# Kernel optimization log

Measured on AMD Instinct MI355X. Metric: run time of the kernel, lower is better.

## Reference

```python
import jax, jax.numpy as jnp
import numpy as np

B, C, H, W = 4, 256, 64, 64
CK = C // 8  # query/key channels per OUT_RATIO=8


def setup_inputs() -> dict:
    key = jax.random.key(0)
    ks = jax.random.split(key, 8)
    s_in = 1.0 / np.sqrt(C)
    return {
        "x": jax.random.normal(ks[0], (B, C, H, W), dtype=jnp.float32),
        "Wq": jax.random.uniform(ks[1], (CK, C), jnp.float32, -s_in, s_in),
        "bq": jax.random.uniform(ks[2], (CK,), jnp.float32, -s_in, s_in),
        "Wk": jax.random.uniform(ks[3], (CK, C), jnp.float32, -s_in, s_in),
        "bk": jax.random.uniform(ks[4], (CK,), jnp.float32, -s_in, s_in),
        "Wv": jax.random.uniform(ks[5], (C, C), jnp.float32, -s_in, s_in),
        "bv": jax.random.uniform(ks[6], (C,), jnp.float32, -s_in, s_in),
        "gamma": jnp.zeros((1,), dtype=jnp.float32),
    }


def reference(x, Wq, bq, Wk, bk, Wv, bv, gamma):
    b, c, h, w = x.shape
    n = h * w
    xf = x.reshape(b, c, n)  # [B, C, N]
    # 1x1 convs are channel matmuls
    q = jnp.einsum('oc,bcn->bno', Wq, xf) + bq  # [B, N, CK]
    k = jnp.einsum('oc,bcn->bon', Wk, xf) + bk[None, :, None]  # [B, CK, N]
    v = jnp.einsum('oc,bcn->bon', Wv, xf) + bv[None, :, None]  # [B, C, N]
    energy = jnp.einsum('bno,bom->bnm', q, k)  # [B, N, N], unscaled
    attn = jax.nn.softmax(energy, axis=-1)
    out = jnp.einsum('bcm,bnm->bcn', v, attn)  # [B, C, N]
    out = out.reshape(b, c, h, w)
    return gamma[0] * out + x
```

## Files before the change

kernel.cpp:

```cpp
#include <hip/hip_runtime.h>
#include <math.h>


#define BB 4
#define CC 256
#define NN 4096
#define CKK 32
#define LOG2E 1.44269504f

typedef __attribute__((ext_vector_type(4))) float f32x4;
typedef __attribute__((ext_vector_type(16))) float f32x16;
typedef __attribute__((ext_vector_type(8))) short short8;
typedef __attribute__((ext_vector_type(4))) short short4v;

static __device__ __forceinline__ ushort f2bf(float f) {
    union { float f; unsigned u; } v; v.f = f;
    unsigned r = v.u + 0x7FFFu + ((v.u >> 16) & 1u);
    return (ushort)(r >> 16);
}
static __device__ __forceinline__ float bf2f(ushort h) {
    union { unsigned u; float f; } v; v.u = ((unsigned)h) << 16;
    return v.f;
}
static __device__ __forceinline__ unsigned pack2(float lo, float hi) {
    unsigned r;
    asm("v_cvt_pk_bf16_f32 %0, %1, %2" : "=v"(r) : "v"(lo), "v"(hi));
    return r;
}
static __device__ __forceinline__ float exp2fast(float x) {
    return __builtin_amdgcn_exp2f(x);
}
static __device__ __forceinline__ void gload_lds16(const void* g, void* l) {
    __builtin_amdgcn_global_load_lds(
        (const __attribute__((address_space(1))) void*)g,
        (__attribute__((address_space(3))) void*)l, 16, 0, 0);
}

__global__ __launch_bounds__(256) void pack_w_kernel(
    const float* __restrict__ Wq, const float* __restrict__ bq,
    const float* __restrict__ Wk, const float* __restrict__ bk,
    const float* __restrict__ Wv, const float* __restrict__ bv,
    ushort* __restrict__ Wb, float* __restrict__ bias)
{
    const int o = blockIdx.x;
    const int c = threadIdx.x;
    const float* src; float bsc;
    if (o < 32)      { src = Wq + o * CC;        bsc = bq[o]; }
    else if (o < 64) { src = Wk + (o - 32) * CC; bsc = bk[o - 32]; }
    else             { src = Wv + (o - 64) * CC; bsc = bv[o - 64]; }
    Wb[o * CC + c] = f2bf(src[c]);
    if (c == 0) bias[o] = bsc;
}

__global__ __launch_bounds__(256) void qkv_mfma_kernel(
    const ushort* __restrict__ Wb, const float* __restrict__ bias,
    const float* __restrict__ x,
    ushort* __restrict__ Q, ushort* __restrict__ Kt, ushort* __restrict__ Vg)
{
    const int b = blockIdx.y, n0 = blockIdx.x * 64;
    const int tid = threadIdx.x;
    const int w = tid >> 6, lane = tid & 63, l15 = lane & 15, q = lane >> 4;

    f32x4 acc[5][4];
    #pragma unroll
    for (int c5 = 0; c5 < 5; ++c5)
        #pragma unroll
        for (int nc = 0; nc < 4; ++nc) acc[c5][nc] = (f32x4)0.f;

    const float* xb = x + (size_t)b * CC * NN + n0;

    #pragma unroll
    for (int ks = 0; ks < 8; ++ks) {
        short8 af[5];
        #pragma unroll
        for (int c5 = 0; c5 < 5; ++c5)
            af[c5] = *(const short8*)&Wb[(w * 80 + c5 * 16 + l15) * CC + ks * 32 + q * 8];
        union { unsigned u[4]; short8 v; } bfu[4];
        #pragma unroll
        for (int nc = 0; nc < 4; ++nc) {
            const float* xp = xb + (size_t)(ks * 32 + q * 8) * NN + nc * 16 + l15;
            bfu[nc].u[0] = pack2(xp[0],              xp[(size_t)NN]);
            bfu[nc].u[1] = pack2(xp[2 * (size_t)NN], xp[3 * (size_t)NN]);
            bfu[nc].u[2] = pack2(xp[4 * (size_t)NN], xp[5 * (size_t)NN]);
            bfu[nc].u[3] = pack2(xp[6 * (size_t)NN], xp[7 * (size_t)NN]);
        }
        #pragma unroll
        for (int c5 = 0; c5 < 5; ++c5)
            #pragma unroll
            for (int nc = 0; nc < 4; ++nc)
                acc[c5][nc] = __builtin_amdgcn_mfma_f32_16x16x32_bf16(af[c5], bfu[nc].v, acc[c5][nc], 0, 0, 0);
    }

    const int kh2b = (l15 >> 2) & 1;
    const int jj   = (l15 & 3) + ((l15 >> 3) << 2);

    #pragma unroll
    for (int c5 = 0; c5 < 5; ++c5) {
        const int o0 = w * 80 + c5 * 16;
        float bia[4];
        #pragma unroll
        for (int r = 0; r < 4; ++r) bia[r] = bias[o0 + q * 4 + r];
        if (o0 >= 64) {
            #pragma unroll
            for (int nc = 0; nc < 4; ++nc) {
                const size_t tbase =
                    ((size_t)b * (NN / 32) + (n0 >> 5) + (nc >> 1)) * 8192
                    + (size_t)(((nc & 1) << 1) + kh2b) * 2048 + jj;
                #pragma unroll
                for (int r = 0; r < 4; ++r) {
                    const int c = o0 - 64 + q * 4 + r;
                    Vg[tbase + c * 8] = f2bf(acc[c5][nc][r] + bia[r]);
                }
            }
        } else {
            ushort* dst = (o0 < 32) ? Q : Kt;
            const float sc = (o0 < 32) ? LOG2E : 1.0f;
            const int oo = (o0 & 31) + q * 4;
            #pragma unroll
            for (int nc = 0; nc < 4; ++nc) {
                short4v h;
                #pragma unroll
                for (int r = 0; r < 4; ++r) h[r] = (short)f2bf((acc[c5][nc][r] + bia[r]) * sc);
                *(short4v*)&dst[((size_t)b * NN + n0 + nc * 16 + l15) * CKK + oo] = h;
            }
        }
    }
}

__global__ __launch_bounds__(256, 2) void attn_mfma_kernel(
    const ushort* __restrict__ Q, const ushort* __restrict__ K,
    const ushort* __restrict__ Vg,
    ushort* __restrict__ Op, float* __restrict__ Mp, float* __restrict__ Lp,
    int G, int NSEG)
{
    __shared__ __align__(16) ushort vs[2][16384];

    const int id = blockIdx.x;
    const int xcd = id & 7, ix = id >> 3;
    const int b = xcd >> 1;
    int g, row;
    if (G == 4) { g = ((xcd & 1) << 1) | (ix & 1); row = ix >> 1; }
    else        { g = xcd & 1;                     row = ix; }
    const int n0 = row * 128;

    const int tid = threadIdx.x;
    const int w = tid >> 6, lane = tid & 63;
    const int l31 = lane & 31, h2 = lane >> 5;
    const int n0w = n0 + w * 32;

    const size_t qrow = ((size_t)b * NN + n0w + l31) * CKK;
    short8 qB0 = *(const short8*)&Q[qrow + h2 * 8];
    short8 qB1 = *(const short8*)&Q[qrow + 16 + h2 * 8];

    f32x16 acc[8];
    #pragma unroll
    for (int cb = 0; cb < 8; ++cb) acc[cb] = (f32x16)0.f;
    float m_i = -3.0e38f, l_p = 0.f;

    const int m_start = g * NSEG;
    const int NT = NSEG / 64;
    const ushort* Kb = K + (size_t)b * NN * CKK;
    const char* Vseg = (const char*)Vg
        + ((size_t)b * (NN / 32) + (size_t)(m_start >> 5)) * 16384;

    const int goff = (w << 10) + (lane << 4);
    const int loff = (w << 10);

    #pragma unroll
    for (int i = 0; i < 8; ++i)
        gload_lds16(Vseg + (i << 12) + goff, (char*)&vs[0][0] + (i << 12) + loff);

    short8 kA0 = *(const short8*)&Kb[(size_t)(m_start + l31) * CKK + h2 * 8];
    short8 kA1 = *(const short8*)&Kb[(size_t)(m_start + l31) * CKK + 16 + h2 * 8];
    f32x16 s = __builtin_amdgcn_mfma_f32_32x32x16_bf16(kA0, qB0, (f32x16)0.f, 0, 0, 0);
    s = __builtin_amdgcn_mfma_f32_32x32x16_bf16(kA1, qB1, s, 0, 0, 0);
    {
        const int m1 = m_start + ((NSEG > 32) ? 32 : 0);
        kA0 = *(const short8*)&Kb[(size_t)(m1 + l31) * CKK + h2 * 8];
        kA1 = *(const short8*)&Kb[(size_t)(m1 + l31) * CKK + 16 + h2 * 8];
    }
    __syncthreads();

    int cur = 0;
    for (int t = 0; t < NT; ++t) {
        const char* Vtn = Vseg + (size_t)((t + 1 < NT) ? t + 1 : 0) * 32768;
        #pragma unroll
        for (int i = 0; i < 8; ++i)
            gload_lds16(Vtn + (i << 12) + goff, (char*)&vs[cur ^ 1][0] + (i << 12) + loff);

        #pragma unroll
        for (int sub = 0; sub < 2; ++sub) {
            const int u = 2 * t + sub;

            f32x16 sn = __builtin_amdgcn_mfma_f32_32x32x16_bf16(kA0, qB0, (f32x16)0.f, 0, 0, 0);
            sn = __builtin_amdgcn_mfma_f32_32x32x16_bf16(kA1, qB1, sn, 0, 0, 0);
            const int mo2 = (u + 2) * 32;
            const int m2 = m_start + ((mo2 < NSEG) ? mo2 : 0);
            kA0 = *(const short8*)&Kb[(size_t)(m2 + l31) * CKK + h2 * 8];
            kA1 = *(const short8*)&Kb[(size_t)(m2 + l31) * CKK + 16 + h2 * 8];

            float t0 = fmaxf(fmaxf(s[0],  s[1]),  s[2]);
            float t1 = fmaxf(fmaxf(s[3],  s[4]),  s[5]);
            float t2 = fmaxf(fmaxf(s[6],  s[7]),  s[8]);
            float t3 = fmaxf(fmaxf(s[9],  s[10]), s[11]);
            float t4 = fmaxf(fmaxf(s[12], s[13]), s[14]);
            float mx = fmaxf(fmaxf(fmaxf(t0, t1), t2), fmaxf(fmaxf(t3, t4), s[15]));
            mx = fmaxf(mx, __shfl_xor(mx, 32));
            const bool resc = mx > m_i + 8.f;
            const float mn = resc ? mx : m_i;
            const float al = resc ? exp2fast(m_i - mx) : 1.f;
            union { unsigned uu[8]; short8 v[2]; } P;
            float sum0 = 0.f, sum1 = 0.f;
            #pragma unroll
            for (int g2 = 0; g2 < 8; ++g2) {
                const float plo = exp2fast(s[2 * g2]     - mn);
                const float phi = exp2fast(s[2 * g2 + 1] - mn);
                if (g2 & 1) sum1 += plo + phi; else sum0 += plo + phi;
                P.uu[g2] = pack2(plo, phi);
            }
            l_p = l_p * al + (sum0 + sum1);
            m_i = mn;
            if (__any(resc)) {
                #pragma unroll
                for (int cb = 0; cb < 8; ++cb) acc[cb] *= al;
            }

            const ushort* vsub = &vs[cur][sub * 8192];
            __builtin_amdgcn_s_setprio(1);
            #pragma unroll
            for (int cb = 0; cb < 8; ++cb) {
                const short8 A0 = *(const short8*)&vsub[(size_t)h2 * 2048       + (cb * 32 + l31) * 8];
                const short8 A1 = *(const short8*)&vsub[(size_t)(2 + h2) * 2048 + (cb * 32 + l31) * 8];
                acc[cb] = __builtin_amdgcn_mfma_f32_32x32x16_bf16(A0, P.v[0], acc[cb], 0, 0, 0);
                acc[cb] = __builtin_amdgcn_mfma_f32_32x32x16_bf16(A1, P.v[1], acc[cb], 0, 0, 0);
            }
            __builtin_amdgcn_s_setprio(0);

            s = sn;
        }
        __syncthreads();
        cur ^= 1;
    }

    float l = l_p + __shfl_xor(l_p, 32);
    const float linv = 1.f / l;
    if (h2 == 0) {
        const size_t idx = (size_t)(g * BB + b) * NN + n0w + l31;
        Mp[idx] = m_i;
        Lp[idx] = l;
    }
    ushort* ob = Op + (size_t)(g * BB + b) * CC * NN;
    #pragma unroll
    for (int cb = 0; cb < 8; ++cb)
        #pragma unroll
        for (int r = 0; r < 16; ++r) {
            const int c = cb * 32 + (r & 3) + 8 * (r >> 2) + 4 * h2;
            ob[(size_t)c * NN + n0w + l31] = f2bf(acc[cb][r] * linv);
        }
}

template<int G>
__global__ __launch_bounds__(256) void combine_kernel(
    const ushort* __restrict__ Op, const float* __restrict__ Mp,
    const float* __restrict__ Lp, const float* __restrict__ x,
    const float* __restrict__ gamma, float* __restrict__ out)
{
    const int gid = blockIdx.x * 256 + threadIdx.x;
    const int grp   = gid & (NN / 8 - 1);
    const int rowid = gid >> 9;
    const int b = rowid >> 8;
    const int c = rowid & (CC - 1);
    const int n0 = grp * 8;

    f32x4 mp[G][2], lp[G][2];
    #pragma unroll
    for (int g = 0; g < G; ++g) {
        const size_t base = (size_t)(g * BB + b) * NN + n0;
        mp[g][0] = *(const f32x4*)&Mp[base];
        mp[g][1] = *(const f32x4*)&Mp[base + 4];
        lp[g][0] = *(const f32x4*)&Lp[base];
        lp[g][1] = *(const f32x4*)&Lp[base + 4];
    }
    float wgt[G][8];
    #pragma unroll
    for (int h = 0; h < 2; ++h) {
        #pragma unroll
        for (int j = 0; j < 4; ++j) {
            float M = -3.0e38f;
            #pragma unroll
            for (int g = 0; g < G; ++g) M = fmaxf(M, mp[g][h][j]);
            float ws = 0.f;
            #pragma unroll
            for (int g = 0; g < G; ++g) {
                const float wv = lp[g][h][j] * exp2fast(mp[g][h][j] - M);
                wgt[g][h * 4 + j] = wv;
                ws += wv;
            }
            const float inv = 1.f / ws;
            #pragma unroll
            for (int g = 0; g < G; ++g) wgt[g][h * 4 + j] *= inv;
        }
    }

    short8 opv[G];
    #pragma unroll
    for (int g = 0; g < G; ++g)
        opv[g] = *(const short8*)&Op[((size_t)(g * BB + b) * CC + c) * NN + n0];

    const size_t xbase = ((size_t)b * CC + c) * NN + n0;
    const f32x4 x0 = *(const f32x4*)&x[xbase];
    const f32x4 x1 = *(const f32x4*)&x[xbase + 4];
    const float gm = gamma[0];

    f32x4 o0, o1;
    #pragma unroll
    for (int j = 0; j < 4; ++j) {
        float a = 0.f, bsum = 0.f;
        #pragma unroll
        for (int g = 0; g < G; ++g) {
            a    += wgt[g][j]     * bf2f((ushort)opv[g][j]);
            bsum += wgt[g][4 + j] * bf2f((ushort)opv[g][4 + j]);
        }
        o0[j] = gm * a + x0[j];
        o1[j] = gm * bsum + x1[j];
    }
    *(f32x4*)&out[xbase]     = o0;
    *(f32x4*)&out[xbase + 4] = o1;
}

extern "C" void kernel_launch(void* const* d_in, const int* in_sizes, int n_in,
                              void* d_out, int out_size, void* d_ws, size_t ws_size,
                              hipStream_t stream) {
    const float* x     = (const float*)d_in[0];
    const float* Wq    = (const float*)d_in[1];
    const float* bq    = (const float*)d_in[2];
    const float* Wk    = (const float*)d_in[3];
    const float* bk    = (const float*)d_in[4];
    const float* Wv    = (const float*)d_in[5];
    const float* bv    = (const float*)d_in[6];
    const float* gamma = (const float*)d_in[7];
    float* out = (float*)d_out;

    char* p = (char*)d_ws;
    ushort* Wb   = (ushort*)(p);
    float*  bias = (float*) (p + 163840);
    ushort* Qb   = (ushort*)(p + 165120);
    ushort* Kb   = (ushort*)(p + 1213696);
    ushort* Vc   = (ushort*)(p + 2262272);
    float*  Mpb  = (float*) (p + 10650880);
    float*  Lpb  = (float*) (p + 10913024);
    ushort* Opb  = (ushort*)(p + 11175168);
    const int G = (ws_size >= (size_t)44729600) ? 4 : 2;

    pack_w_kernel<<<dim3(320), 256, 0, stream>>>(Wq, bq, Wk, bk, Wv, bv, Wb, bias);
    qkv_mfma_kernel<<<dim3(NN / 64, BB), 256, 0, stream>>>(Wb, bias, x, Qb, Kb, Vc);
    attn_mfma_kernel<<<dim3(128 * G), 256, 0, stream>>>(Qb, Kb, Vc, Opb, Mpb, Lpb, G, NN / G);
    const int cblocks = BB * CC * (NN / 8) / 256;
    if (G == 4)
        combine_kernel<4><<<dim3(cblocks), 256, 0, stream>>>(Opb, Mpb, Lpb, x, gamma, out);
    else
        combine_kernel<2><<<dim3(cblocks), 256, 0, stream>>>(Opb, Mpb, Lpb, x, gamma, out);
}
```

Baseline: 88.21 us.

## Software-pipeline softmax of next tile with PV MFMAs of previous tile

Restructures the flash-attention inner loop so the softmax (exp, max, pack) for sub-tile u+1 is computed before the PV MFMAs for sub-tile u. This lets VALU/transcendental work overlap with matrix-core work instead of serialising. It adds a prologue and epilogue, drops the s_setprio hints, and keeps two P buffers live, which raises register pressure. The rescale of acc is applied after the PV step using the newer alpha, which preserves correctness.

```diff
diff --git a/kernel.cpp b/kernel.cpp
--- a/kernel.cpp
+++ b/kernel.cpp
@@ -34,6 +34,45 @@
     __builtin_amdgcn_global_load_lds(
         (const __attribute__((address_space(1))) void*)g,
         (__attribute__((address_space(3))) void*)l, 16, 0, 0);
+}
+
+union PU { unsigned u[8]; short8 v[2]; };
+
+static __device__ __forceinline__ void softmax_step(
+    const f32x16 s, float& m_i, float& l_p, PU& P, float& al, bool& resc)
+{
+    float t0 = fmaxf(fmaxf(s[0],  s[1]),  s[2]);
+    float t1 = fmaxf(fmaxf(s[3],  s[4]),  s[5]);
+    float t2 = fmaxf(fmaxf(s[6],  s[7]),  s[8]);
+    float t3 = fmaxf(fmaxf(s[9],  s[10]), s[11]);
+    float t4 = fmaxf(fmaxf(s[12], s[13]), s[14]);
+    float mx = fmaxf(fmaxf(fmaxf(t0, t1), t2), fmaxf(fmaxf(t3, t4), s[15]));
+    mx = fmaxf(mx, __shfl_xor(mx, 32));
+    resc = mx > m_i + 8.f;
+    const float mn = resc ? mx : m_i;
+    al = resc ? exp2fast(m_i - mx) : 1.f;
+    float sum0 = 0.f, sum1 = 0.f;
+    #pragma unroll
+    for (int g2 = 0; g2 < 8; ++g2) {
+        const float plo = exp2fast(s[2 * g2]     - mn);
+        const float phi = exp2fast(s[2 * g2 + 1] - mn);
+        if (g2 & 1) sum1 += plo + phi; else sum0 += plo + phi;
+        P.u[g2] = pack2(plo, phi);
+    }
+    l_p = l_p * al + (sum0 + sum1);
+    m_i = mn;
+}
+
+static __device__ __forceinline__ void pv_step(
+    const ushort* vsub, const PU& P, f32x16 (&acc)[8], int h2, int l31)
+{
+    #pragma unroll
+    for (int cb = 0; cb < 8; ++cb) {
+        const short8 A0 = *(const short8*)&vsub[(size_t)h2 * 2048       + (cb * 32 + l31) * 8];
+        const short8 A1 = *(const short8*)&vsub[(size_t)(2 + h2) * 2048 + (cb * 32 + l31) * 8];
+        acc[cb] = __builtin_amdgcn_mfma_f32_32x32x16_bf16(A0, P.v[0], acc[cb], 0, 0, 0);
+        acc[cb] = __builtin_amdgcn_mfma_f32_32x32x16_bf16(A1, P.v[1], acc[cb], 0, 0, 0);
+    }
 }
 
 __global__ __launch_bounds__(256) void pack_w_kernel(
@@ -149,8 +188,8 @@
     const int n0w = n0 + w * 32;
 
     const size_t qrow = ((size_t)b * NN + n0w + l31) * CKK;
-    short8 qB0 = *(const short8*)&Q[qrow + h2 * 8];
-    short8 qB1 = *(const short8*)&Q[qrow + 16 + h2 * 8];
+    const short8 qB0 = *(const short8*)&Q[qrow + h2 * 8];
+    const short8 qB1 = *(const short8*)&Q[qrow + 16 + h2 * 8];
 
     f32x16 acc[8];
     #pragma unroll
@@ -166,80 +205,72 @@
     const int goff = (w << 10) + (lane << 4);
     const int loff = (w << 10);
 
+    PU Pp, Pc; float alp, alc; bool rp, rc;
+
     #pragma unroll
     for (int i = 0; i < 8; ++i)
         gload_lds16(Vseg + (i << 12) + goff, (char*)&vs[0][0] + (i << 12) + loff);
 
     short8 kA0 = *(const short8*)&Kb[(size_t)(m_start + l31) * CKK + h2 * 8];
     short8 kA1 = *(const short8*)&Kb[(size_t)(m_start + l31) * CKK + 16 + h2 * 8];
-    f32x16 s = __builtin_amdgcn_mfma_f32_32x32x16_bf16(kA0, qB0, (f32x16)0.f, 0, 0, 0);
-    s = __builtin_amdgcn_mfma_f32_32x32x16_bf16(kA1, qB1, s, 0, 0, 0);
     {
-        const int m1 = m_start + ((NSEG > 32) ? 32 : 0);
-        kA0 = *(const short8*)&Kb[(size_t)(m1 + l31) * CKK + h2 * 8];
-        kA1 = *(const short8*)&Kb[(size_t)(m1 + l31) * CKK + 16 + h2 * 8];
-    }
-    __syncthreads();
-
-    int cur = 0;
-    for (int t = 0; t < NT; ++t) {
-        const char* Vtn = Vseg + (size_t)((t + 1 < NT) ? t + 1 : 0) * 32768;
+        f32x16 s = __builtin_amdgcn_mfma_f32_32x32x16_bf16(kA0, qB0, (f32x16)0.f, 0, 0, 0);
+        s = __builtin_amdgcn_mfma_f32_32x32x16_bf16(kA1, qB1, s, 0, 0, 0);
+        const size_t kr = (size_t)(m_start + 32 + l31) * CKK;
+        kA0 = *(const short8*)&Kb[kr + h2 * 8];
+        kA1 = *(const short8*)&Kb[kr + 16 + h2 * 8];
+        softmax_step(s, m_i, l_p, Pp, alp, rp);
+    }
+
+    for (int t = 0; t < NT - 1; ++t) {
+        __syncthreads();
+        const char* Vtn = Vseg + (size_t)(t + 1) * 32768;
         #pragma unroll
         for (int i = 0; i < 8; ++i)
-            gload_lds16(Vtn + (i << 12) + goff, (char*)&vs[cur ^ 1][0] + (i << 12) + loff);
-
-        #pragma unroll
-        for (int sub = 0; sub < 2; ++sub) {
-            const int u = 2 * t + sub;
-
+            gload_lds16(Vtn + (i << 12) + goff,
+                        (char*)&vs[(t + 1) & 1][0] + (i << 12) + loff);
+        const ushort* vb = &vs[t & 1][0];
+
+        {
             f32x16 sn = __builtin_amdgcn_mfma_f32_32x32x16_bf16(kA0, qB0, (f32x16)0.f, 0, 0, 0);
             sn = __builtin_amdgcn_mfma_f32_32x32x16_bf16(kA1, qB1, sn, 0, 0, 0);
-            const int mo2 = (u + 2) * 32;
-            const int m2 = m_start + ((mo2 < NSEG) ? mo2 : 0);
-            kA0 = *(const short8*)&Kb[(size_t)(m2 + l31) * CKK + h2 * 8];
-            kA1 = *(const short8*)&Kb[(size_t)(m2 + l31) * CKK + 16 + h2 * 8];
-
-            float t0 = fmaxf(fmaxf(s[0],  s[1]),  s[2]);
-            float t1 = fmaxf(fmaxf(s[3],  s[4]),  s[5]);
-            float t2 = fmaxf(fmaxf(s[6],  s[7]),  s[8]);
-            float t3 = fmaxf(fmaxf(s[9],  s[10]), s[11]);
-            float t4 = fmaxf(fmaxf(s[12], s[13]), s[14]);
-            float mx = fmaxf(fmaxf(fmaxf(t0, t1), t2), fmaxf(fmaxf(t3, t4), s[15]));
-            mx = fmaxf(mx, __shfl_xor(mx, 32));
-            const bool resc = mx > m_i + 8.f;
-            const float mn = resc ? mx : m_i;
-            const float al = resc ? exp2fast(m_i - mx) : 1.f;
-            union { unsigned uu[8]; short8 v[2]; } P;
-            float sum0 = 0.f, sum1 = 0.f;
-            #pragma unroll
-            for (int g2 = 0; g2 < 8; ++g2) {
-                const float plo = exp2fast(s[2 * g2]     - mn);
-                const float phi = exp2fast(s[2 * g2 + 1] - mn);
-                if (g2 & 1) sum1 += plo + phi; else sum0 += plo + phi;
-                P.uu[g2] = pack2(plo, phi);
-            }
-            l_p = l_p * al + (sum0 + sum1);
-            m_i = mn;
-            if (__any(resc)) {
+            const size_t kr = (size_t)(m_start + (2 * t + 2) * 32 + l31) * CKK;
+            kA0 = *(const short8*)&Kb[kr + h2 * 8];
+            kA1 = *(const short8*)&Kb[kr + 16 + h2 * 8];
+            softmax_step(sn, m_i, l_p, Pc, alc, rc);
+            pv_step(vb, Pp, acc, h2, l31);
+            if (__any(rc)) {
                 #pragma unroll
-                for (int cb = 0; cb < 8; ++cb) acc[cb] *= al;
-            }
-
-            const ushort* vsub = &vs[cur][sub * 8192];
-            __builtin_amdgcn_s_setprio(1);
-            #pragma unroll
-            for (int cb = 0; cb < 8; ++cb) {
-                const short8 A0 = *(const short8*)&vsub[(size_t)h2 * 2048       + (cb * 32 + l31) * 8];
-                const short8 A1 = *(const short8*)&vsub[(size_t)(2 + h2) * 2048 + (cb * 32 + l31) * 8];
-                acc[cb] = __builtin_amdgcn_mfma_f32_32x32x16_bf16(A0, P.v[0], acc[cb], 0, 0, 0);
-                acc[cb] = __builtin_amdgcn_mfma_f32_32x32x16_bf16(A1, P.v[1], acc[cb], 0, 0, 0);
-            }
-            __builtin_amdgcn_s_setprio(0);
-
-            s = sn;
-        }
-        __syncthreads();
-        cur ^= 1;
+                for (int cb = 0; cb < 8; ++cb) acc[cb] *= alc;
+            }
+        }
+        {
+            f32x16 sn = __builtin_amdgcn_mfma_f32_32x32x16_bf16(kA0, qB0, (f32x16)0.f, 0, 0, 0);
+            sn = __builtin_amdgcn_mfma_f32_32x32x16_bf16(kA1, qB1, sn, 0, 0, 0);
+            const size_t kr = (size_t)(m_start + (2 * t + 3) * 32 + l31) * CKK;
+            kA0 = *(const short8*)&Kb[kr + h2 * 8];
+            kA1 = *(const short8*)&Kb[kr + 16 + h2 * 8];
+            softmax_step(sn, m_i, l_p, Pp, alp, rp);
+            pv_step(vb + 8192, Pc, acc, h2, l31);
+            if (__any(rp)) {
+                #pragma unroll
+                for (int cb = 0; cb < 8; ++cb) acc[cb] *= alp;
+            }
+        }
+    }
+
+    __syncthreads();
+    {
+        const ushort* vb = &vs[(NT - 1) & 1][0];
+        f32x16 sn = __builtin_amdgcn_mfma_f32_32x32x16_bf16(kA0, qB0, (f32x16)0.f, 0, 0, 0);
+        sn = __builtin_amdgcn_mfma_f32_32x32x16_bf16(kA1, qB1, sn, 0, 0, 0);
+        softmax_step(sn, m_i, l_p, Pc, alc, rc);
+        pv_step(vb, Pp, acc, h2, l31);
+        if (__any(rc)) {
+            #pragma unroll
+            for (int cb = 0; cb < 8; ++cb) acc[cb] *= alc;
+        }
+        pv_step(vb + 8192, Pc, acc, h2, l31);
     }
 
     float l = l_p + __shfl_xor(l_p, 32);
```

After: 85.42 us. 1.03x faster.
